# Optimization experiments

Measured on AMD Instinct MI355X. Metric: run time of the kernel, lower is better.

## Reference

```python
import jax, jax.numpy as jnp
import numpy as np
from jax import lax

B, Hs, Ws = 2, 256, 256
DIM = 256        # query channels (c)
DIM_BAK = 256    # key/value channels (c2)
HEADS = 8
WIN = 8
HEAD_DIM = DIM // HEADS
SCALE = HEAD_DIM ** -0.5


def window_partition(x, ws):
    # x: [B, H, W, C] -> [B*nH*nW, ws, ws, C]
    b, h, w, c = x.shape
    x = x.reshape(b, h // ws, ws, w // ws, ws, c)
    return x.transpose(0, 1, 3, 2, 4, 5).reshape(-1, ws, ws, c)


def window_reverse(windows, ws, h, w):
    # windows: [B*nH*nW, ws, ws, C] -> [B, H, W, C]
    b = windows.shape[0] // ((h // ws) * (w // ws))
    x = windows.reshape(b, h // ws, w // ws, ws, ws, -1)
    return x.transpose(0, 1, 3, 2, 4, 5).reshape(b, h, w, -1)


def setup_inputs() -> dict:
    key = jax.random.key(0)
    ks = jax.random.split(key, 9)
    s = 0.02
    return {
        "query_feature": jax.random.normal(ks[0], (B, DIM, Hs, Ws), jnp.float32),
        "key_value_feature": jax.random.normal(ks[1], (B, DIM_BAK, Hs, Ws), jnp.float32),
        # depthwise 3x3 conv on kv (groups=DIM_BAK, bias=False): OIHW with I=1
        "w_dw": jax.random.normal(ks[2], (DIM_BAK, 1, 3, 3), jnp.float32) * s,
        # to_q: Linear(dim -> dim), stored [in, out]
        "wq": jax.random.normal(ks[3], (DIM, DIM), jnp.float32) * s,
        "bq": jax.random.normal(ks[4], (DIM,), jnp.float32) * s,
        # to_kv: Linear(dim_bak -> 2*dim)
        "wkv": jax.random.normal(ks[5], (DIM_BAK, 2 * DIM), jnp.float32) * s,
        "bkv": jax.random.normal(ks[6], (2 * DIM,), jnp.float32) * s,
        # project_out: Linear(dim -> dim)
        "w_proj": jax.random.normal(ks[7], (DIM, DIM), jnp.float32) * s,
        "b_proj": jax.random.normal(ks[8], (DIM,), jnp.float32) * s,
    }


def reference(query_feature, key_value_feature, w_dw, wq, bq, wkv, bkv, w_proj, b_proj):
    b, c, h, w = query_feature.shape
    c2 = key_value_feature.shape[1]

    # depthwise 3x3 conv on key/value feature (padding=1, stride=1)
    kv = lax.conv_general_dilated(
        key_value_feature, w_dw,
        window_strides=(1, 1), padding="SAME",
        feature_group_count=c2,
        dimension_numbers=("NCHW", "OIHW", "NCHW"))

    # NCHW -> NHWC, partition into non-overlapping windows
    qw = window_partition(query_feature.transpose(0, 2, 3, 1), WIN)  # [B_, ws, ws, c]
    kvw = window_partition(kv.transpose(0, 2, 3, 1), WIN)            # [B_, ws, ws, c2]
    B_ = qw.shape[0]
    N = WIN * WIN
    qw = qw.reshape(B_, N, c)
    kvw = kvw.reshape(B_, N, c2)

    # projections -> multi-head [B_, heads, N, head_dim]
    q = (qw @ wq + bq).reshape(B_, N, HEADS, HEAD_DIM).transpose(0, 2, 1, 3) * SCALE
    kv_proj = (kvw @ wkv + bkv).reshape(B_, N, 2, HEADS, HEAD_DIM)
    k = kv_proj[:, :, 0].transpose(0, 2, 1, 3)
    v = kv_proj[:, :, 1].transpose(0, 2, 1, 3)

    # windowed cross-attention
    attn = jax.nn.softmax(jnp.einsum("bhnd,bhmd->bhnm", q, k), axis=-1)
    out = jnp.einsum("bhnm,bhmd->bhnd", attn, v)
    out = out.transpose(0, 2, 1, 3).reshape(B_, N, c)
    out = out @ w_proj + b_proj

    # reverse windows, back to NCHW
    out = window_reverse(out.reshape(B_, WIN, WIN, c), WIN, h, w)
    return out.transpose(0, 3, 1, 2)
```

## Files before the change

kernel.cpp:

```cpp
#include <hip/hip_runtime.h>
#include <hip/hip_bf16.h>
#include <cstdint>
#include <cstddef>

typedef __hip_bfloat16 bf16;
typedef short bf16x8 __attribute__((ext_vector_type(8)));
typedef float f32x4 __attribute__((ext_vector_type(4)));

#define MFMA(a, b, c) __builtin_amdgcn_mfma_f32_16x16x32_bf16((a), (b), (c), 0, 0, 0)

__global__ __launch_bounds__(256) void wtrans_k(const float* __restrict__ wq,
                                                const float* __restrict__ wkv,
                                                const float* __restrict__ wp,
                                                bf16* __restrict__ wqT,
                                                bf16* __restrict__ wkvT,
                                                bf16* __restrict__ wpT) {
  int idx = blockIdx.x * 256 + threadIdx.x;
  if (idx < 65536) {
    int n = idx >> 8, k = idx & 255;
    wqT[idx] = __float2bfloat16(wq[k * 256 + n]);
  } else if (idx < 196608) {
    int i = idx - 65536;
    int n = i >> 8, k = i & 255;
    wkvT[i] = __float2bfloat16(wkv[k * 512 + n]);
  } else {
    int i = idx - 196608;
    int n = i >> 8, k = i & 255;
    wpT[i] = __float2bfloat16(wp[k * 256 + n]);
  }
}

__global__ __launch_bounds__(256) void t_winq_k(const float* __restrict__ src,
                                                bf16* __restrict__ dst,
                                                int hw0, int swoff) {
  __shared__ bf16 T[64][66];
  int tile = blockIdx.x;
  int c0 = (tile & 3) << 6;
  int hwb = hw0 + ((tile >> 2) << 6);
  int tid = threadIdx.x;
  {
    int hwl = tid & 63, cb = tid >> 6;
    const float* s = src + (size_t)(c0 + cb) * 65536 + hwb + hwl;
#pragma unroll
    for (int i = 0; i < 16; ++i)
      T[cb + i * 4][hwl] = __float2bfloat16(s[(size_t)i * 4 * 65536]);
  }
  __syncthreads();
  {
    int cl = tid & 63, hb = tid >> 6;
#pragma unroll
    for (int j = 0; j < 16; ++j) {
      int hwl = hb + j * 4;
      int hw = hwb + hwl;
      int h = hw >> 8, w = hw & 255;
      int sw = swoff + ((h >> 3) << 5) + (w >> 3);
      int t = ((h & 7) << 3) + (w & 7);
      dst[((size_t)(sw * 64 + t) << 8) + c0 + cl] = T[cl][hwl];
    }
  }
}

__global__ __launch_bounds__(256) void t_nhwc_k(const float* __restrict__ src,
                                                bf16* __restrict__ dst) {
  __shared__ bf16 T[64][66];
  int tile = blockIdx.x;
  int c0 = (tile & 3) << 6;
  int hwoff = (tile >> 2) << 6;
  int tid = threadIdx.x;
  {
    int hwl = tid & 63, cb = tid >> 6;
    const float* s = src + (size_t)(c0 + cb) * 65536 + hwoff + hwl;
#pragma unroll
    for (int i = 0; i < 16; ++i)
      T[cb + i * 4][hwl] = __float2bfloat16(s[(size_t)i * 4 * 65536]);
  }
  __syncthreads();
  {
    int cl = tid & 63, hb = tid >> 6;
#pragma unroll
    for (int j = 0; j < 16; ++j) {
      int hwl = hb + j * 4;
      dst[((size_t)(hwoff + hwl) << 8) + c0 + cl] = T[cl][hwl];
    }
  }
}

__global__ __launch_bounds__(256) void convkv_k(const bf16* __restrict__ SK,
                                                const float* __restrict__ wdw,
                                                const bf16* __restrict__ wkvT,
                                                const float* __restrict__ bkv,
                                                bf16* __restrict__ k_s,
                                                bf16* __restrict__ vT_s,
                                                int wid_base, int cnt, int psw0,
                                                int nwtot) {
  __shared__ __align__(16) bf16 X[64 * 256];
  auto xp = [&](int row, int col) -> bf16* {
    int by = (row << 9) + (col << 1);
    by ^= (row & 7) << 4;
    return (bf16*)((char*)X + by);
  };
  int bid = blockIdx.x;
  int swc = (bid & 7) * (cnt >> 3) + (bid >> 3);
  int sw = psw0 + swc;
  int wid = wid_base + swc;
  int rem = wid & 1023, wh = rem >> 5, ww = rem & 31;
  int h0 = wh * 8, w0 = ww * 8;
  int tid = threadIdx.x;
  {
    int c = tid;
    float wr[9];
#pragma unroll
    for (int q = 0; q < 9; ++q) wr[q] = wdw[c * 9 + q];
    const bool wlo = (w0 > 0), whi = (w0 < 248);
    float rows[3][10];
    auto load_row = [&](int gh, float* r) {
      if (gh >= 0 && gh < 256) {
        const bf16* rp = SK + ((size_t)(gh * 256 + w0) << 8) + c;
        r[0] = wlo ? __bfloat162float(rp[-256]) : 0.f;
#pragma unroll
        for (int s = 1; s <= 8; ++s) r[s] = __bfloat162float(rp[(s - 1) * 256]);
        r[9] = whi ? __bfloat162float(rp[8 * 256]) : 0.f;
      } else {
#pragma unroll
        for (int e = 0; e < 10; ++e) r[e] = 0.f;
      }
    };
    load_row(h0 - 1, rows[0]);
    load_row(h0, rows[1]);
#pragma unroll
    for (int i = 0; i < 8; ++i) {
      load_row(h0 + i + 1, rows[(i + 2) % 3]);
#pragma unroll
      for (int j = 0; j < 8; ++j) {
        float acc = 0.f;
#pragma unroll
        for (int di = 0; di < 3; ++di) {
          const float* rp = rows[(i + di) % 3];
          acc = __builtin_fmaf(wr[di * 3 + 0], rp[j], acc);
          acc = __builtin_fmaf(wr[di * 3 + 1], rp[j + 1], acc);
          acc = __builtin_fmaf(wr[di * 3 + 2], rp[j + 2], acc);
        }
        *xp(i * 8 + j, c) = __float2bfloat16(acc);
      }
    }
  }
  __syncthreads();
  int wave = tid >> 6, lane = tid & 63, quad = lane >> 4, l16 = lane & 15;
  int n0 = wave * 64;
  f32x4 zero4 = {0.f, 0.f, 0.f, 0.f};
  f32x4 acc[4][4];
  for (int mt = 0; mt < 4; ++mt)
    for (int nt = 0; nt < 4; ++nt) acc[mt][nt] = zero4;
  for (int k0 = 0; k0 < 256; k0 += 32) {
    bf16x8 a[4], bb[4];
    for (int mt = 0; mt < 4; ++mt)
      a[mt] = *(const bf16x8*)xp(mt * 16 + l16, k0 + quad * 8);
    for (int nt = 0; nt < 4; ++nt)
      bb[nt] = *(const bf16x8*)&wkvT[(size_t)(n0 + nt * 16 + l16) * 256 + k0 + quad * 8];
    for (int mt = 0; mt < 4; ++mt)
      for (int nt = 0; nt < 4; ++nt) acc[mt][nt] = MFMA(a[mt], bb[nt], acc[mt][nt]);
  }
  for (int nt = 0; nt < 4; ++nt) {
    int n = n0 + nt * 16 + l16;
    float bias = bkv[n];
    for (int mt = 0; mt < 4; ++mt) {
      int mb = mt * 16 + quad * 4;
      for (int r = 0; r < 4; ++r)
        k_s[((size_t)(sw * 64 + mb + r) << 8) + n] =
            __float2bfloat16(acc[mt][nt][r] + bias);
    }
  }
  for (int mt = 0; mt < 4; ++mt)
    for (int nt = 0; nt < 4; ++nt) acc[mt][nt] = zero4;
  for (int k0 = 0; k0 < 256; k0 += 32) {
    bf16x8 a[4], bb[4];
    for (int mt = 0; mt < 4; ++mt)
      a[mt] = *(const bf16x8*)xp(mt * 16 + l16, k0 + quad * 8);
    for (int nt = 0; nt < 4; ++nt)
      bb[nt] = *(const bf16x8*)&wkvT[(size_t)(256 + n0 + nt * 16 + l16) * 256 + k0 + quad * 8];
    for (int mt = 0; mt < 4; ++mt)
      for (int nt = 0; nt < 4; ++nt) acc[mt][nt] = MFMA(bb[nt], a[mt], acc[mt][nt]);
  }
  for (int nt = 0; nt < 4; ++nt) {
    for (int r = 0; r < 4; ++r) {
      int vd = n0 + nt * 16 + quad * 4 + r;
      float bias = bkv[256 + vd];
      for (int mt = 0; mt < 4; ++mt)
        vT_s[((size_t)(sw * 256 + vd) << 6) + mt * 16 + l16] =
            __float2bfloat16(acc[mt][nt][r] + bias);
    }
  }
}

__global__ __launch_bounds__(256, 2) void fused_k(const bf16* __restrict__ qwM,
                                                  const bf16* __restrict__ wqT,
                                                  const float* __restrict__ bq,
                                                  const bf16* __restrict__ k_s,
                                                  const bf16* __restrict__ vT_s,
                                                  const bf16* __restrict__ wpT,
                                                  const float* __restrict__ bp,
                                                  float* __restrict__ out,
                                                  int wid_base, int nw) {
  __shared__ __align__(16) bf16 XQ[64 * 256];
  int bid = blockIdx.x;
  int sw = (bid & 7) * (nw >> 3) + (bid >> 3);
  int wid = wid_base + sw;
  int b = wid >> 10, rem = wid & 1023, wh = rem >> 5, ww = rem & 31;
  int h0 = wh * 8, w0 = ww * 8;
  int tid = threadIdx.x, wave = tid >> 6, lane = tid & 63, quad = lane >> 4, l16 = lane & 15;
  const bf16* kw = k_s + ((size_t)sw << 14);
  const bf16* vw = vT_s + ((size_t)sw << 14);

  {
    const char* Aq = (const char*)(qwM + ((size_t)sw << 14));
#pragma unroll
    for (int rr = 0; rr < 8; ++rr) {
      int L = rr * 4096 + wave * 1024 + lane * 16;
      int gl = L ^ (((L >> 9) & 7) << 4);
      __builtin_amdgcn_global_load_lds(
          (const __attribute__((address_space(1))) void*)(Aq + gl),
          (__attribute__((address_space(3))) void*)((char*)XQ + rr * 4096 + wave * 1024),
          16, 0, 0);
    }
  }
  bf16x8 kfr[2][4], vfr[2][2][2];
#pragma unroll
  for (int hi = 0; hi < 2; ++hi) {
    int co = (wave + hi * 4) * 32;
#pragma unroll
    for (int nt = 0; nt < 4; ++nt)
      kfr[hi][nt] = *(const bf16x8*)&kw[(size_t)(nt * 16 + l16) * 256 + co + quad * 8];
#pragma unroll
    for (int half = 0; half < 2; ++half)
#pragma unroll
      for (int nt = 0; nt < 2; ++nt)
        vfr[hi][half][nt] =
            *(const bf16x8*)&vw[(size_t)(co + nt * 16 + l16) * 64 + half * 32 + quad * 8];
  }
  __syncthreads();

  auto xq = [&](int row, int col) -> const bf16* {
    int by = (row << 9) + (col << 1);
    by ^= (row & 7) << 4;
    return (const bf16*)((const char*)XQ + by);
  };
  char* Abase = (char*)XQ + wave * 8192;
  auto ap = [&](int row, int col) -> bf16* {
    int by = (row << 7) + (col << 1);
    by ^= (row & 7) << 4;
    return (bf16*)(Abase + by);
  };
  auto apR = [&](int w, int row, int col) -> bf16* {
    int by = (row << 7) + (col << 1);
    by ^= (row & 7) << 4;
    return (bf16*)((char*)XQ + w * 8192 + by);
  };
  f32x4 zero4 = {0.f, 0.f, 0.f, 0.f};

  f32x4 qacc[4][4];
  for (int mt = 0; mt < 4; ++mt)
    for (int nt = 0; nt < 4; ++nt) qacc[mt][nt] = zero4;
  for (int k0 = 0; k0 < 256; k0 += 32) {
    bf16x8 a[4], bb[4];
    for (int mt = 0; mt < 4; ++mt)
      a[mt] = *(const bf16x8*)xq(mt * 16 + l16, k0 + quad * 8);
    for (int nt = 0; nt < 4; ++nt) {
      int n = (wave + ((nt >> 1) << 2)) * 32 + (nt & 1) * 16 + l16;
      bb[nt] = *(const bf16x8*)&wqT[(size_t)n * 256 + k0 + quad * 8];
    }
    for (int mt = 0; mt < 4; ++mt)
      for (int nt = 0; nt < 4; ++nt) qacc[mt][nt] = MFMA(a[mt], bb[nt], qacc[mt][nt]);
  }
  __syncthreads();
  {
    const float scale = 0.1767766952966369f;
    for (int nt = 0; nt < 4; ++nt) {
      int n = (wave + ((nt >> 1) << 2)) * 32 + (nt & 1) * 16 + l16;
      float bias = bq[n];
      for (int mt = 0; mt < 4; ++mt) {
        int mb = mt * 16 + quad * 4;
        for (int r = 0; r < 4; ++r)
          *ap(mb + r, nt * 16 + l16) =
              __float2bfloat16((qacc[mt][nt][r] + bias) * scale);
      }
    }
  }
#pragma unroll
  for (int hi = 0; hi < 2; ++hi) {
    int lc = hi * 32;
    f32x4 s[4][4];
    for (int mt = 0; mt < 4; ++mt)
      for (int nt = 0; nt < 4; ++nt) s[mt][nt] = zero4;
    {
      bf16x8 a[4];
      for (int mt = 0; mt < 4; ++mt)
        a[mt] = *(const bf16x8*)ap(mt * 16 + l16, lc + quad * 8);
      for (int mt = 0; mt < 4; ++mt)
#pragma unroll
        for (int nt = 0; nt < 4; ++nt) s[mt][nt] = MFMA(a[mt], kfr[hi][nt], s[mt][nt]);
    }
    float rsum[4][4];
    for (int mt = 0; mt < 4; ++mt) {
      for (int r = 0; r < 4; ++r) {
        float m = s[mt][0][r];
        for (int nt = 1; nt < 4; ++nt) m = fmaxf(m, s[mt][nt][r]);
        m = fmaxf(m, __shfl_xor(m, 1, 64));
        m = fmaxf(m, __shfl_xor(m, 2, 64));
        m = fmaxf(m, __shfl_xor(m, 4, 64));
        m = fmaxf(m, __shfl_xor(m, 8, 64));
        float sum = 0.f;
        for (int nt = 0; nt < 4; ++nt) {
          float e = __expf(s[mt][nt][r] - m);
          s[mt][nt][r] = e;
          sum += e;
        }
        sum += __shfl_xor(sum, 1, 64);
        sum += __shfl_xor(sum, 2, 64);
        sum += __shfl_xor(sum, 4, 64);
        sum += __shfl_xor(sum, 8, 64);
        rsum[mt][r] = sum;
      }
    }
    f32x4 o[4][2];
    for (int mt = 0; mt < 4; ++mt)
      for (int nt = 0; nt < 2; ++nt) o[mt][nt] = zero4;
#pragma unroll
    for (int half = 0; half < 2; ++half) {
      for (int mt = 0; mt < 4; ++mt)
#pragma unroll
        for (int nt2 = 0; nt2 < 2; ++nt2)
          for (int r = 0; r < 4; ++r)
            *ap(mt * 16 + quad * 4 + r, lc + nt2 * 16 + l16) =
                __float2bfloat16(s[mt][half * 2 + nt2][r]);
      bf16x8 pa[4];
      for (int mt = 0; mt < 4; ++mt)
        pa[mt] = *(const bf16x8*)ap(mt * 16 + l16, lc + quad * 8);
      for (int mt = 0; mt < 4; ++mt)
#pragma unroll
        for (int nt = 0; nt < 2; ++nt)
          o[mt][nt] = MFMA(pa[mt], vfr[hi][half][nt], o[mt][nt]);
    }
    for (int mt = 0; mt < 4; ++mt) {
      int mb = mt * 16 + quad * 4;
      for (int nt = 0; nt < 2; ++nt)
        for (int r = 0; r < 4; ++r)
          *ap(mb + r, lc + nt * 16 + l16) =
              __float2bfloat16(o[mt][nt][r] / rsum[mt][r]);
    }
  }
  __syncthreads();
  {
    int n0 = wave * 64;
    f32x4 acc[4][4];
    for (int mt = 0; mt < 4; ++mt)
      for (int nt = 0; nt < 4; ++nt) acc[mt][nt] = zero4;
    for (int k0 = 0; k0 < 256; k0 += 32) {
      int head = k0 >> 5;
      int rw = head & 3;
      int lc = (head >> 2) * 32;
      bf16x8 a[4], bb[4];
      for (int mt = 0; mt < 4; ++mt)
        a[mt] = *(const bf16x8*)apR(rw, mt * 16 + l16, lc + quad * 8);
      for (int nt = 0; nt < 4; ++nt)
        bb[nt] = *(const bf16x8*)&wpT[(size_t)(n0 + nt * 16 + l16) * 256 + k0 + quad * 8];
      for (int mt = 0; mt < 4; ++mt)
        for (int nt = 0; nt < 4; ++nt) acc[mt][nt] = MFMA(a[mt], bb[nt], acc[mt][nt]);
    }
    for (int nt = 0; nt < 4; ++nt) {
      int n = n0 + nt * 16 + l16;
      float bias = bp[n];
      float* chan = out + ((size_t)(b * 256 + n) << 16);
      for (int mt = 0; mt < 4; ++mt) {
        int row_i = mt * 2 + (quad >> 1);
        int j0 = (quad & 1) * 4;
        f32x4 v4;
        for (int r = 0; r < 4; ++r) v4[r] = acc[mt][nt][r] + bias;
        *(f32x4*)&chan[(size_t)(h0 + row_i) * 256 + w0 + j0] = v4;
      }
    }
  }
}

extern "C" void kernel_launch(void* const* d_in, const int* in_sizes, int n_in,
                              void* d_out, int out_size, void* d_ws, size_t ws_size,
                              hipStream_t stream) {
  const float* qf  = (const float*)d_in[0];
  const float* kvf = (const float*)d_in[1];
  const float* wdw = (const float*)d_in[2];
  const float* wq  = (const float*)d_in[3];
  const float* bq  = (const float*)d_in[4];
  const float* wkv = (const float*)d_in[5];
  const float* bkv = (const float*)d_in[6];
  const float* wp  = (const float*)d_in[7];
  const float* bp  = (const float*)d_in[8];
  float* out = (float*)d_out;

  bf16* wqT  = (bf16*)d_ws;
  bf16* wkvT = wqT + 65536;
  bf16* wpT  = wkvT + 131072;
  bf16* bufs = wpT + 65536;
  const size_t welems = 65536 + 131072 + 65536;
  const size_t skelems = (size_t)256 * 256 * 256;

  int passes = 1;
  while (passes < 32) {
    size_t nw_ = 2048 / passes;
    size_t elems = welems + skelems + 3 * nw_ * 16384;
    if (elems * 2 <= ws_size) break;
    passes <<= 1;
  }
  int nw = 2048 / passes;
  size_t sz = (size_t)nw * 16384;
  bf16* SK  = bufs;
  bf16* qwM = SK + skelems;
  bf16* KS  = qwM + sz;
  bf16* VT  = KS + sz;

  wtrans_k<<<1024, 256, 0, stream>>>(wq, wkv, wp, wqT, wkvT, wpT);

  for (int p = 0; p < passes; ++p) {
    int wbP = p * nw;
    int b0 = wbP >> 10, b1 = (wbP + nw - 1) >> 10;
    for (int b = b0; b <= b1; ++b) {
      int s = wbP > b * 1024 ? wbP : b * 1024;
      int e = (wbP + nw) < (b + 1) * 1024 ? (wbP + nw) : (b + 1) * 1024;
      int cnt = e - s;
      int h0 = ((s & 1023) >> 5) * 8;
      t_winq_k<<<cnt * 4, 256, 0, stream>>>(qf + ((size_t)b << 24), qwM,
                                            h0 * 256, b * 1024 - wbP);
    }
    for (int b = b0; b <= b1; ++b) {
      int s = wbP > b * 1024 ? wbP : b * 1024;
      int e = (wbP + nw) < (b + 1) * 1024 ? (wbP + nw) : (b + 1) * 1024;
      int cnt = e - s;
      t_nhwc_k<<<4096, 256, 0, stream>>>(kvf + ((size_t)b << 24), SK);
      convkv_k<<<cnt, 256, 0, stream>>>(SK, wdw, wkvT, bkv, KS, VT,
                                        s, cnt, s - wbP, nw);
    }
    fused_k<<<nw, 256, 0, stream>>>(qwM, wqT, bq, KS, VT, wpT, bp, out, wbP, nw);
  }
}
```

Measured before the change: 598.3 us.

## Merge staging kernels and run whole batch in one pass when workspace fits

Adds a combined stage_k kernel that does the weight transpose, the query window layout and the kv NHWC transpose in one launch. When the workspace is large enough, the host now runs the whole batch in three launches instead of a per-batch loop with many small launches, using a per-batch SK buffer selected via a mask. It also wraps the attention MFMA blocks with s_setprio to favour matrix issue. The cost is a larger workspace requirement and extra code paths for the smaller-workspace fallbacks.

```diff
diff --git a/kernel.cpp b/kernel.cpp
--- a/kernel.cpp
+++ b/kernel.cpp
@@ -8,6 +8,89 @@
 typedef float f32x4 __attribute__((ext_vector_type(4)));
 
 #define MFMA(a, b, c) __builtin_amdgcn_mfma_f32_16x16x32_bf16((a), (b), (c), 0, 0, 0)
+
+__global__ __launch_bounds__(256) void stage_k(
+    const float* __restrict__ wq, const float* __restrict__ wkv,
+    const float* __restrict__ wp, bf16* __restrict__ wqT,
+    bf16* __restrict__ wkvT, bf16* __restrict__ wpT,
+    const float* __restrict__ qf, bf16* __restrict__ qwM,
+    const float* __restrict__ kvf, bf16* __restrict__ SK,
+    int b0, int nb, int skmask, int wbP, int do_w) {
+  __shared__ bf16 T[64][66];
+  int bid = blockIdx.x;
+  int tid = threadIdx.x;
+  int wb = do_w ? 1024 : 0;
+  if (bid < wb) {
+    int idx = bid * 256 + tid;
+    if (idx < 65536) {
+      int n = idx >> 8, k = idx & 255;
+      wqT[idx] = __float2bfloat16(wq[k * 256 + n]);
+    } else if (idx < 196608) {
+      int i = idx - 65536;
+      int n = i >> 8, k = i & 255;
+      wkvT[i] = __float2bfloat16(wkv[k * 512 + n]);
+    } else {
+      int i = idx - 196608;
+      int n = i >> 8, k = i & 255;
+      wpT[i] = __float2bfloat16(wp[k * 256 + n]);
+    }
+    return;
+  }
+  int tile = bid - wb;
+  int qtiles = nb * 4096;
+  if (tile < qtiles) {
+    int b = b0 + (tile >> 12);
+    int t = tile & 4095;
+    int c0 = (t & 3) << 6;
+    int hwb = (t >> 2) << 6;
+    const float* src = qf + ((size_t)b << 24);
+    {
+      int hwl = tid & 63, cb = tid >> 6;
+      const float* s = src + (size_t)(c0 + cb) * 65536 + hwb + hwl;
+#pragma unroll
+      for (int i = 0; i < 16; ++i)
+        T[cb + i * 4][hwl] = __float2bfloat16(s[(size_t)i * 4 * 65536]);
+    }
+    __syncthreads();
+    {
+      int cl = tid & 63, hb = tid >> 6;
+      int swoff = b * 1024 - wbP;
+#pragma unroll
+      for (int j = 0; j < 16; ++j) {
+        int hwl = hb + j * 4;
+        int hw = hwb + hwl;
+        int h = hw >> 8, w = hw & 255;
+        int sw = swoff + ((h >> 3) << 5) + (w >> 3);
+        int tt = ((h & 7) << 3) + (w & 7);
+        qwM[((size_t)(sw * 64 + tt) << 8) + c0 + cl] = T[cl][hwl];
+      }
+    }
+  } else {
+    tile -= qtiles;
+    int b = b0 + (tile >> 12);
+    int t = tile & 4095;
+    int c0 = (t & 3) << 6;
+    int hwoff = (t >> 2) << 6;
+    const float* src = kvf + ((size_t)b << 24);
+    bf16* dst = SK + (size_t)(b & skmask) * 16777216;
+    {
+      int hwl = tid & 63, cb = tid >> 6;
+      const float* s = src + (size_t)(c0 + cb) * 65536 + hwoff + hwl;
+#pragma unroll
+      for (int i = 0; i < 16; ++i)
+        T[cb + i * 4][hwl] = __float2bfloat16(s[(size_t)i * 4 * 65536]);
+    }
+    __syncthreads();
+    {
+      int cl = tid & 63, hb = tid >> 6;
+#pragma unroll
+      for (int j = 0; j < 16; ++j) {
+        int hwl = hb + j * 4;
+        dst[((size_t)(hwoff + hwl) << 8) + c0 + cl] = T[cl][hwl];
+      }
+    }
+  }
+}
 
 __global__ __launch_bounds__(256) void wtrans_k(const float* __restrict__ wq,
                                                 const float* __restrict__ wkv,
@@ -92,7 +175,7 @@
                                                 bf16* __restrict__ k_s,
                                                 bf16* __restrict__ vT_s,
                                                 int wid_base, int cnt, int psw0,
-                                                int nwtot) {
+                                                int skmask) {
   __shared__ __align__(16) bf16 X[64 * 256];
   auto xp = [&](int row, int col) -> bf16* {
     int by = (row << 9) + (col << 1);
@@ -103,8 +186,10 @@
   int swc = (bid & 7) * (cnt >> 3) + (bid >> 3);
   int sw = psw0 + swc;
   int wid = wid_base + swc;
+  int b = wid >> 10;
   int rem = wid & 1023, wh = rem >> 5, ww = rem & 31;
   int h0 = wh * 8, w0 = ww * 8;
+  const bf16* SKb = SK + (size_t)(b & skmask) * 16777216;
   int tid = threadIdx.x;
   {
     int c = tid;
@@ -115,7 +200,7 @@
     float rows[3][10];
     auto load_row = [&](int gh, float* r) {
       if (gh >= 0 && gh < 256) {
-        const bf16* rp = SK + ((size_t)(gh * 256 + w0) << 8) + c;
+        const bf16* rp = SKb + ((size_t)(gh * 256 + w0) << 8) + c;
         r[0] = wlo ? __bfloat162float(rp[-256]) : 0.f;
 #pragma unroll
         for (int s = 1; s <= 8; ++s) r[s] = __bfloat162float(rp[(s - 1) * 256]);
@@ -295,9 +380,11 @@
       bf16x8 a[4];
       for (int mt = 0; mt < 4; ++mt)
         a[mt] = *(const bf16x8*)ap(mt * 16 + l16, lc + quad * 8);
+      __builtin_amdgcn_s_setprio(1);
       for (int mt = 0; mt < 4; ++mt)
 #pragma unroll
         for (int nt = 0; nt < 4; ++nt) s[mt][nt] = MFMA(a[mt], kfr[hi][nt], s[mt][nt]);
+      __builtin_amdgcn_s_setprio(0);
     }
     float rsum[4][4];
     for (int mt = 0; mt < 4; ++mt) {
@@ -335,10 +422,12 @@
       bf16x8 pa[4];
       for (int mt = 0; mt < 4; ++mt)
         pa[mt] = *(const bf16x8*)ap(mt * 16 + l16, lc + quad * 8);
+      __builtin_amdgcn_s_setprio(1);
       for (int mt = 0; mt < 4; ++mt)
 #pragma unroll
         for (int nt = 0; nt < 2; ++nt)
           o[mt][nt] = MFMA(pa[mt], vfr[hi][half][nt], o[mt][nt]);
+      __builtin_amdgcn_s_setprio(0);
     }
     for (int mt = 0; mt < 4; ++mt) {
       int mb = mt * 16 + quad * 4;
@@ -400,24 +489,55 @@
   bf16* wpT  = wkvT + 131072;
   bf16* bufs = wpT + 65536;
   const size_t welems = 65536 + 131072 + 65536;
-  const size_t skelems = (size_t)256 * 256 * 256;
-
-  int passes = 1;
-  while (passes < 32) {
-    size_t nw_ = 2048 / passes;
-    size_t elems = welems + skelems + 3 * nw_ * 16384;
-    if (elems * 2 <= ws_size) break;
+  const size_t skel = (size_t)256 * 256 * 256;
+
+  size_t fitelems = welems + 2 * skel + (size_t)3 * 2048 * 16384;
+  if (fitelems * 2 <= ws_size) {
+    bf16* SK  = bufs;
+    bf16* qwM = SK + 2 * skel;
+    bf16* KS  = qwM + (size_t)2048 * 16384;
+    bf16* VT  = KS + (size_t)2048 * 16384;
+    stage_k<<<1024 + 2 * 4096 * 2, 256, 0, stream>>>(
+        wq, wkv, wp, wqT, wkvT, wpT, qf, qwM, kvf, SK,
+        0, 2, 1, 0, 1);
+    convkv_k<<<2048, 256, 0, stream>>>(SK, wdw, wkvT, bkv, KS, VT,
+                                       0, 2048,
+                                       0, 1);
+    fused_k<<<2048, 256, 0, stream>>>(qwM, wqT, bq, KS, VT, wpT, bp, out,
+                                      0, 2048);
+    return;
+  }
+
+  size_t midelems = welems + skel + (size_t)3 * 1024 * 16384;
+  if (midelems * 2 <= ws_size) {
+    bf16* SK  = bufs;
+    bf16* qwM = SK + skel;
+    bf16* KS  = qwM + (size_t)1024 * 16384;
+    bf16* VT  = KS + (size_t)1024 * 16384;
+    wtrans_k<<<1024, 256, 0, stream>>>(wq, wkv, wp, wqT, wkvT, wpT);
+    for (int b = 0; b < 2; ++b) {
+      stage_k<<<2 * 4096, 256, 0, stream>>>(
+          wq, wkv, wp, wqT, wkvT, wpT, qf, qwM, kvf, SK,
+          b, 1, 0, b * 1024, 0);
+      convkv_k<<<1024, 256, 0, stream>>>(SK, wdw, wkvT, bkv, KS, VT,
+                                         b * 1024, 1024, 0, 0);
+      fused_k<<<1024, 256, 0, stream>>>(qwM, wqT, bq, KS, VT, wpT, bp, out,
+                                        b * 1024, 1024);
+    }
+    return;
+  }
+
+  int passes = 4;
+  while (passes < 32 &&
+         (welems + skel + (size_t)3 * (2048 / passes) * 16384) * 2 > ws_size)
     passes <<= 1;
-  }
   int nw = 2048 / passes;
   size_t sz = (size_t)nw * 16384;
   bf16* SK  = bufs;
-  bf16* qwM = SK + skelems;
+  bf16* qwM = SK + skel;
   bf16* KS  = qwM + sz;
   bf16* VT  = KS + sz;
-
   wtrans_k<<<1024, 256, 0, stream>>>(wq, wkv, wp, wqT, wkvT, wpT);
-
   for (int p = 0; p < passes; ++p) {
     int wbP = p * nw;
     int b0 = wbP >> 10, b1 = (wbP + nw - 1) >> 10;
@@ -428,14 +548,9 @@
       int h0 = ((s & 1023) >> 5) * 8;
       t_winq_k<<<cnt * 4, 256, 0, stream>>>(qf + ((size_t)b << 24), qwM,
                                             h0 * 256, b * 1024 - wbP);
-    }
-    for (int b = b0; b <= b1; ++b) {
-      int s = wbP > b * 1024 ? wbP : b * 1024;
-      int e = (wbP + nw) < (b + 1) * 1024 ? (wbP + nw) : (b + 1) * 1024;
-      int cnt = e - s;
       t_nhwc_k<<<4096, 256, 0, stream>>>(kvf + ((size_t)b << 24), SK);
       convkv_k<<<cnt, 256, 0, stream>>>(SK, wdw, wkvT, bkv, KS, VT,
-                                        s, cnt, s - wbP, nw);
+                                        s, cnt, s - wbP, 0);
     }
     fused_k<<<nw, 256, 0, stream>>>(qwM, wqT, bq, KS, VT, wpT, bp, out, wbP, nw);
   }
```

After: 589.0 us. About the same (-1.6%).

## Merge stages into one multi-role kernel and overlap batches across launches

Applied to the files above, without the earlier changes.

Turns the separate weight-transpose, staging, conv+KV-projection and fused attention kernels into device functions dispatched by block index inside one pipe_k kernel. When the workspace is large enough, batch 1 staging runs in the same launch as batch 0 conv, and batch 1 conv runs alongside batch 0 fused attention. This cuts launch count and fills idle CUs at stage boundaries. It also adds s_setprio around the MFMA loops in attention. In exchange, the kernel loses launch_bounds(256,2) on the fused path, which can change register allocation and occupancy, and it needs a larger workspace for both batches.

```diff
diff --git a/kernel.cpp b/kernel.cpp
--- a/kernel.cpp
+++ b/kernel.cpp
@@ -9,13 +9,10 @@
 
 #define MFMA(a, b, c) __builtin_amdgcn_mfma_f32_16x16x32_bf16((a), (b), (c), 0, 0, 0)
 
-__global__ __launch_bounds__(256) void wtrans_k(const float* __restrict__ wq,
-                                                const float* __restrict__ wkv,
-                                                const float* __restrict__ wp,
-                                                bf16* __restrict__ wqT,
-                                                bf16* __restrict__ wkvT,
-                                                bf16* __restrict__ wpT) {
-  int idx = blockIdx.x * 256 + threadIdx.x;
+
+__device__ __forceinline__ void d_wtrans(int idx, const float* wq,
+                                         const float* wkv, const float* wp,
+                                         bf16* wqT, bf16* wkvT, bf16* wpT) {
   if (idx < 65536) {
     int n = idx >> 8, k = idx & 255;
     wqT[idx] = __float2bfloat16(wq[k * 256 + n]);
@@ -30,14 +27,11 @@
   }
 }
 
-__global__ __launch_bounds__(256) void t_winq_k(const float* __restrict__ src,
-                                                bf16* __restrict__ dst,
-                                                int hw0, int swoff) {
-  __shared__ bf16 T[64][66];
-  int tile = blockIdx.x;
+__device__ __forceinline__ void d_stageq(int tile, int tid, const float* src,
+                                         bf16* qwM, int swoff, char* SMEM) {
+  bf16(*T)[66] = (bf16(*)[66])SMEM;
   int c0 = (tile & 3) << 6;
-  int hwb = hw0 + ((tile >> 2) << 6);
-  int tid = threadIdx.x;
+  int hwb = (tile >> 2) << 6;
   {
     int hwl = tid & 63, cb = tid >> 6;
     const float* s = src + (size_t)(c0 + cb) * 65536 + hwb + hwl;
@@ -54,19 +48,17 @@
       int hw = hwb + hwl;
       int h = hw >> 8, w = hw & 255;
       int sw = swoff + ((h >> 3) << 5) + (w >> 3);
-      int t = ((h & 7) << 3) + (w & 7);
-      dst[((size_t)(sw * 64 + t) << 8) + c0 + cl] = T[cl][hwl];
-    }
-  }
-}
-
-__global__ __launch_bounds__(256) void t_nhwc_k(const float* __restrict__ src,
-                                                bf16* __restrict__ dst) {
-  __shared__ bf16 T[64][66];
-  int tile = blockIdx.x;
+      int tt = ((h & 7) << 3) + (w & 7);
+      qwM[((size_t)(sw * 64 + tt) << 8) + c0 + cl] = T[cl][hwl];
+    }
+  }
+}
+
+__device__ __forceinline__ void d_stagekv(int tile, int tid, const float* src,
+                                          bf16* dst, char* SMEM) {
+  bf16(*T)[66] = (bf16(*)[66])SMEM;
   int c0 = (tile & 3) << 6;
   int hwoff = (tile >> 2) << 6;
-  int tid = threadIdx.x;
   {
     int hwl = tid & 63, cb = tid >> 6;
     const float* s = src + (size_t)(c0 + cb) * 65536 + hwoff + hwl;
@@ -85,27 +77,24 @@
   }
 }
 
-__global__ __launch_bounds__(256) void convkv_k(const bf16* __restrict__ SK,
-                                                const float* __restrict__ wdw,
-                                                const bf16* __restrict__ wkvT,
-                                                const float* __restrict__ bkv,
-                                                bf16* __restrict__ k_s,
-                                                bf16* __restrict__ vT_s,
-                                                int wid_base, int cnt, int psw0,
-                                                int nwtot) {
-  __shared__ __align__(16) bf16 X[64 * 256];
+__device__ __forceinline__ void d_convkv(int ib, int cnt, int wid_base,
+                                         int bufoff, int skmask, int tid,
+                                         const bf16* SK, const float* wdw,
+                                         const bf16* wkvT, const float* bkv,
+                                         bf16* k_s, bf16* vT_s, char* SMEM) {
+  bf16* X = (bf16*)SMEM;
   auto xp = [&](int row, int col) -> bf16* {
     int by = (row << 9) + (col << 1);
     by ^= (row & 7) << 4;
     return (bf16*)((char*)X + by);
   };
-  int bid = blockIdx.x;
-  int swc = (bid & 7) * (cnt >> 3) + (bid >> 3);
-  int sw = psw0 + swc;
+  int swc = (ib & 7) * (cnt >> 3) + (ib >> 3);
   int wid = wid_base + swc;
+  int gw = wid - bufoff;
+  int b = wid >> 10;
   int rem = wid & 1023, wh = rem >> 5, ww = rem & 31;
   int h0 = wh * 8, w0 = ww * 8;
-  int tid = threadIdx.x;
+  const bf16* SKb = SK + (size_t)(b & skmask) * 16777216;
   {
     int c = tid;
     float wr[9];
@@ -115,7 +104,7 @@
     float rows[3][10];
     auto load_row = [&](int gh, float* r) {
       if (gh >= 0 && gh < 256) {
-        const bf16* rp = SK + ((size_t)(gh * 256 + w0) << 8) + c;
+        const bf16* rp = SKb + ((size_t)(gh * 256 + w0) << 8) + c;
         r[0] = wlo ? __bfloat162float(rp[-256]) : 0.f;
 #pragma unroll
         for (int s = 1; s <= 8; ++s) r[s] = __bfloat162float(rp[(s - 1) * 256]);
@@ -166,7 +155,7 @@
     for (int mt = 0; mt < 4; ++mt) {
       int mb = mt * 16 + quad * 4;
       for (int r = 0; r < 4; ++r)
-        k_s[((size_t)(sw * 64 + mb + r) << 8) + n] =
+        k_s[((size_t)(gw * 64 + mb + r) << 8) + n] =
             __float2bfloat16(acc[mt][nt][r] + bias);
     }
   }
@@ -186,40 +175,38 @@
       int vd = n0 + nt * 16 + quad * 4 + r;
       float bias = bkv[256 + vd];
       for (int mt = 0; mt < 4; ++mt)
-        vT_s[((size_t)(sw * 256 + vd) << 6) + mt * 16 + l16] =
+        vT_s[((size_t)(gw * 256 + vd) << 6) + mt * 16 + l16] =
             __float2bfloat16(acc[mt][nt][r] + bias);
     }
   }
 }
 
-__global__ __launch_bounds__(256, 2) void fused_k(const bf16* __restrict__ qwM,
-                                                  const bf16* __restrict__ wqT,
-                                                  const float* __restrict__ bq,
-                                                  const bf16* __restrict__ k_s,
-                                                  const bf16* __restrict__ vT_s,
-                                                  const bf16* __restrict__ wpT,
-                                                  const float* __restrict__ bp,
-                                                  float* __restrict__ out,
-                                                  int wid_base, int nw) {
-  __shared__ __align__(16) bf16 XQ[64 * 256];
-  int bid = blockIdx.x;
-  int sw = (bid & 7) * (nw >> 3) + (bid >> 3);
+__device__ __forceinline__ void d_fused(int ib, int nw, int wid_base,
+                                        int bufoff, int tid,
+                                        const bf16* qwM, const bf16* wqT,
+                                        const float* bq, const bf16* k_s,
+                                        const bf16* vT_s, const bf16* wpT,
+                                        const float* bp, float* out,
+                                        char* SMEM) {
+  bf16* XQ = (bf16*)SMEM;
+  int sw = (ib & 7) * (nw >> 3) + (ib >> 3);
   int wid = wid_base + sw;
+  int gw = wid - bufoff;
   int b = wid >> 10, rem = wid & 1023, wh = rem >> 5, ww = rem & 31;
   int h0 = wh * 8, w0 = ww * 8;
-  int tid = threadIdx.x, wave = tid >> 6, lane = tid & 63, quad = lane >> 4, l16 = lane & 15;
-  const bf16* kw = k_s + ((size_t)sw << 14);
-  const bf16* vw = vT_s + ((size_t)sw << 14);
-
-  {
-    const char* Aq = (const char*)(qwM + ((size_t)sw << 14));
+  int wave = tid >> 6, lane = tid & 63, quad = lane >> 4, l16 = lane & 15;
+  const bf16* kw = k_s + ((size_t)gw << 14);
+  const bf16* vw = vT_s + ((size_t)gw << 14);
+
+  {
+    const char* Aq = (const char*)(qwM + ((size_t)gw << 14));
 #pragma unroll
     for (int rr = 0; rr < 8; ++rr) {
       int L = rr * 4096 + wave * 1024 + lane * 16;
       int gl = L ^ (((L >> 9) & 7) << 4);
       __builtin_amdgcn_global_load_lds(
           (const __attribute__((address_space(1))) void*)(Aq + gl),
-          (__attribute__((address_space(3))) void*)((char*)XQ + rr * 4096 + wave * 1024),
+          (__attribute__((address_space(3))) void*)(SMEM + rr * 4096 + wave * 1024),
           16, 0, 0);
     }
   }
@@ -295,9 +282,11 @@
       bf16x8 a[4];
       for (int mt = 0; mt < 4; ++mt)
         a[mt] = *(const bf16x8*)ap(mt * 16 + l16, lc + quad * 8);
+      __builtin_amdgcn_s_setprio(1);
       for (int mt = 0; mt < 4; ++mt)
 #pragma unroll
         for (int nt = 0; nt < 4; ++nt) s[mt][nt] = MFMA(a[mt], kfr[hi][nt], s[mt][nt]);
+      __builtin_amdgcn_s_setprio(0);
     }
     float rsum[4][4];
     for (int mt = 0; mt < 4; ++mt) {
@@ -335,10 +324,12 @@
       bf16x8 pa[4];
       for (int mt = 0; mt < 4; ++mt)
         pa[mt] = *(const bf16x8*)ap(mt * 16 + l16, lc + quad * 8);
+      __builtin_amdgcn_s_setprio(1);
       for (int mt = 0; mt < 4; ++mt)
 #pragma unroll
         for (int nt = 0; nt < 2; ++nt)
           o[mt][nt] = MFMA(pa[mt], vfr[hi][half][nt], o[mt][nt]);
+      __builtin_amdgcn_s_setprio(0);
     }
     for (int mt = 0; mt < 4; ++mt) {
       int mb = mt * 16 + quad * 4;
@@ -378,6 +369,46 @@
         *(f32x4*)&chan[(size_t)(h0 + row_i) * 256 + w0 + j0] = v4;
       }
     }
+  }
+}
+
+__global__ __launch_bounds__(256) void pipe_k(
+    int do_w, int nconv, int conv_wb, int nfused, int fused_wb,
+    int nsq, const float* sqsrc, int sq_swoff,
+    int nskv, const float* skvsrc, bf16* skvdst,
+    int bufoff, int skmask,
+    const float* wq, const float* wkv, const float* wp,
+    bf16* wqT, bf16* wkvT, bf16* wpT,
+    const bf16* SK, const float* wdw, const float* bkv,
+    bf16* qwM, const float* bq,
+    bf16* KS, bf16* VT, const float* bp, float* out) {
+  __shared__ __align__(16) char SMEM[32768];
+  int bid = blockIdx.x, tid = threadIdx.x;
+  int wb = do_w ? 1024 : 0;
+  if (bid < wb) {
+    d_wtrans(bid * 256 + tid, wq, wkv, wp, wqT, wkvT, wpT);
+    return;
+  }
+  bid -= wb;
+  if (bid < nconv) {
+    d_convkv(bid, nconv, conv_wb, bufoff, skmask, tid, SK, wdw, wkvT, bkv, KS,
+             VT, SMEM);
+    return;
+  }
+  bid -= nconv;
+  if (bid < nfused) {
+    d_fused(bid, nfused, fused_wb, bufoff, tid, qwM, wqT, bq, KS, VT, wpT, bp,
+            out, SMEM);
+    return;
+  }
+  bid -= nfused;
+  if (bid < nsq) {
+    d_stageq(bid, tid, sqsrc, qwM, sq_swoff, SMEM);
+    return;
+  }
+  bid -= nsq;
+  if (bid < nskv) {
+    d_stagekv(bid, tid, skvsrc, skvdst, SMEM);
   }
 }
 
@@ -400,43 +431,52 @@
   bf16* wpT  = wkvT + 131072;
   bf16* bufs = wpT + 65536;
   const size_t welems = 65536 + 131072 + 65536;
-  const size_t skelems = (size_t)256 * 256 * 256;
-
-  int passes = 1;
-  while (passes < 32) {
-    size_t nw_ = 2048 / passes;
-    size_t elems = welems + skelems + 3 * nw_ * 16384;
-    if (elems * 2 <= ws_size) break;
-    passes <<= 1;
-  }
-  int nw = 2048 / passes;
-  size_t sz = (size_t)nw * 16384;
-  bf16* SK  = bufs;
-  bf16* qwM = SK + skelems;
-  bf16* KS  = qwM + sz;
-  bf16* VT  = KS + sz;
-
-  wtrans_k<<<1024, 256, 0, stream>>>(wq, wkv, wp, wqT, wkvT, wpT);
-
-  for (int p = 0; p < passes; ++p) {
-    int wbP = p * nw;
-    int b0 = wbP >> 10, b1 = (wbP + nw - 1) >> 10;
-    for (int b = b0; b <= b1; ++b) {
-      int s = wbP > b * 1024 ? wbP : b * 1024;
-      int e = (wbP + nw) < (b + 1) * 1024 ? (wbP + nw) : (b + 1) * 1024;
-      int cnt = e - s;
-      int h0 = ((s & 1023) >> 5) * 8;
-      t_winq_k<<<cnt * 4, 256, 0, stream>>>(qf + ((size_t)b << 24), qwM,
-                                            h0 * 256, b * 1024 - wbP);
-    }
-    for (int b = b0; b <= b1; ++b) {
-      int s = wbP > b * 1024 ? wbP : b * 1024;
-      int e = (wbP + nw) < (b + 1) * 1024 ? (wbP + nw) : (b + 1) * 1024;
-      int cnt = e - s;
-      t_nhwc_k<<<4096, 256, 0, stream>>>(kvf + ((size_t)b << 24), SK);
-      convkv_k<<<cnt, 256, 0, stream>>>(SK, wdw, wkvT, bkv, KS, VT,
-                                        s, cnt, s - wbP, nw);
-    }
-    fused_k<<<nw, 256, 0, stream>>>(qwM, wqT, bq, KS, VT, wpT, bp, out, wbP, nw);
-  }
-}
+  const size_t skel = (size_t)256 * 256 * 256;
+
+  const float* q0 = qf;
+  const float* q1 = qf + ((size_t)1 << 24);
+  const float* k0 = kvf;
+  const float* k1 = kvf + ((size_t)1 << 24);
+
+  size_t fitelems = welems + 2 * skel + (size_t)3 * 2048 * 16384;
+  if (fitelems * 2 <= ws_size) {
+    bf16* SK  = bufs;
+    bf16* qwM = SK + 2 * skel;
+    bf16* KS  = qwM + (size_t)2048 * 16384;
+    bf16* VT  = KS + (size_t)2048 * 16384;
+    pipe_k<<<1024 + 4096 + 4096, 256, 0, stream>>>(
+        1, 0, 0, 0, 0, 4096, q0, 0, 4096, k0, SK, 0, 1,
+        wq, wkv, wp, wqT, wkvT, wpT, SK, wdw, bkv, qwM, bq, KS, VT, bp, out);
+    pipe_k<<<1024 + 4096 + 4096, 256, 0, stream>>>(
+        0, 1024, 0, 0, 0, 4096, q1, 1024, 4096, k1, SK + skel, 0, 1,
+        wq, wkv, wp, wqT, wkvT, wpT, SK, wdw, bkv, qwM, bq, KS, VT, bp, out);
+    pipe_k<<<2048, 256, 0, stream>>>(
+        0, 1024, 1024, 1024, 0, 0, q0, 0, 0, k0, SK, 0, 1,
+        wq, wkv, wp, wqT, wkvT, wpT, SK, wdw, bkv, qwM, bq, KS, VT, bp, out);
+    pipe_k<<<1024, 256, 0, stream>>>(
+        0, 0, 0, 1024, 1024, 0, q0, 0, 0, k0, SK, 0, 1,
+        wq, wkv, wp, wqT, wkvT, wpT, SK, wdw, bkv, qwM, bq, KS, VT, bp, out);
+    return;
+  }
+
+  {
+    bf16* SK  = bufs;
+    bf16* qwM = SK + skel;
+    bf16* KS  = qwM + (size_t)1024 * 16384;
+    bf16* VT  = KS + (size_t)1024 * 16384;
+    for (int b = 0; b < 2; ++b) {
+      const float* qb = b ? q1 : q0;
+      const float* kb = b ? k1 : k0;
+      int bo = b * 1024;
+      pipe_k<<<(b == 0 ? 1024 : 0) + 4096 + 4096, 256, 0, stream>>>(
+          b == 0 ? 1 : 0, 0, 0, 0, 0, 4096, qb, 0, 4096, kb, SK, bo, 0,
+          wq, wkv, wp, wqT, wkvT, wpT, SK, wdw, bkv, qwM, bq, KS, VT, bp, out);
+      pipe_k<<<1024, 256, 0, stream>>>(
+          0, 1024, bo, 0, 0, 0, qb, 0, 0, kb, SK, bo, 0,
+          wq, wkv, wp, wqT, wkvT, wpT, SK, wdw, bkv, qwM, bq, KS, VT, bp, out);
+      pipe_k<<<1024, 256, 0, stream>>>(
+          0, 0, 0, 1024, bo, 0, qb, 0, 0, kb, SK, bo, 0,
+          wq, wkv, wp, wqT, wkvT, wpT, SK, wdw, bkv, qwM, bq, KS, VT, bp, out);
+    }
+  }
+}
```

After: 707.2 us. 1.18x slower.
